# Kernel tuning notes

Measured on AMD Instinct MI355X. Metric: run time of the kernel, lower is better.

The kernel has to match this reference:

```python
import jax, jax.numpy as jnp
import numpy as np
from jax import lax

G = 64      # ngroup
CPN = 4     # channels per group in hidden layers
H, W = 32, 64
K = 5       # conv kernel
BIN = 8     # bin_num
BIAS = 3.5  # (bin_num-1)/2
NMIX = 3    # GMM components (batch replicas)
SCALE = 65536.0


def _group_mask(cout, cin, strict):
    # wavefront causality: tap (dg, di, dj) allowed iff dg+di+dj < 0 (strict) or <= 0
    g = jnp.arange(G)
    dg = g[None, :] - g[:, None]                      # (Gout, Gin)
    off = jnp.arange(K) - K // 2
    dd = off[:, None] + off[None, :]                  # (K, K)
    tot = dg[:, :, None, None] + dd[None, None, :, :]
    m = (tot < 0) if strict else (tot <= 0)
    m = jnp.repeat(jnp.repeat(m, cout, axis=0), cin, axis=1)
    return m.astype(jnp.float32)                      # (G*cout, G*cin, K, K)


def _cconv(x, w, b, m, relu):
    y = lax.conv_general_dilated(x, w * m, (1, 1), 'SAME',
                                 dimension_numbers=('NCHW', 'OIHW', 'NCHW'))
    y = y + b[None, :, None, None]
    return jax.nn.relu(y) if relu else y


def setup_inputs() -> dict:
    key = jax.random.key(0)
    ks = jax.random.split(key, 8)
    data = jax.random.randint(ks[0], (1, G, H, W), 0, BIN).astype(jnp.float32)
    mask = jax.random.randint(ks[1], (1, G, H, W), 0, 2).astype(jnp.float32)
    s = 0.05
    w_in = jax.random.normal(ks[2], (G * CPN, G, K, K), jnp.float32) * s
    b_in = jnp.zeros((G * CPN,), jnp.float32)
    w_hid = jax.random.normal(ks[3], (10, G * CPN, G * CPN, K, K), jnp.float32) * s
    b_hid = jnp.zeros((10, G * CPN), jnp.float32)
    w_out = jax.random.normal(ks[4], (G * NMIX, G * CPN, K, K), jnp.float32) * s
    b_out = jnp.zeros((G * NMIX,), jnp.float32)
    return dict(data=data, mask=mask, w_in=w_in, b_in=b_in,
                w_hid=w_hid, b_hid=b_hid, w_out=w_out, b_out=b_out)


def reference(data, mask, w_in, b_in, w_hid, b_hid, w_out, b_out):
    m_in = _group_mask(CPN, 1, True)      # first layer: strict (excludes current group)
    m_hid = _group_mask(CPN, CPN, False)
    m_out = _group_mask(NMIX, CPN, False)
    tdata = (data - BIAS) * mask
    x = jnp.concatenate([tdata, tdata, tdata], axis=0)   # (3, G, H, W)
    x = _cconv(x, w_in, b_in, m_in, True)
    for i in range(5):                                   # 5 residual blocks
        h = _cconv(x, w_hid[2 * i], b_hid[2 * i], m_hid, True)
        h = _cconv(h, w_hid[2 * i + 1], b_hid[2 * i + 1], m_hid, True)
        x = x + h
    y = _cconv(x, w_out, b_out, m_out, False)            # (3, G*3, H, W)
    y = y.reshape(NMIX, G, NMIX, H, W)                   # batch replica m -> mixture m
    logits = y[:, :, 0]
    mu = y[:, :, 1]
    sig = jax.nn.softplus(y[:, :, 2]) + 1e-6
    wts = jax.nn.softmax(logits, axis=0)                 # (3, G, H, W)
    edges = jnp.arange(BIN, dtype=jnp.float32) + 0.5 - BIAS
    z = (edges[:, None, None, None, None] - mu[None]) / (sig[None] * jnp.float32(np.sqrt(2.0)))
    cdf = 0.5 * (1.0 + lax.erf(z))                       # (BIN, 3, G, H, W)
    table = jnp.einsum('kmghw,mghw->ghwk', cdf, wts) * SCALE
    return table                                         # (G, H, W, BIN) quantizable CDF
```

## Files before the change

### kernel.cpp

```cpp
#include <hip/hip_runtime.h>
#include <math.h>

typedef _Float16 f16;
typedef _Float16 f16x8 __attribute__((ext_vector_type(8)));
typedef float f32x4 __attribute__((ext_vector_type(4)));

#define HH 32
#define WW 64
#define NPX 2048
#define SLOTS 68
#define LOSCALE 2048.0f
#define INV_LOSCALE 4.8828125e-4f

typedef const __attribute__((address_space(1))) void gvoid;
typedef __attribute__((address_space(3))) void lvoid;
__device__ __forceinline__ void gload_lds16(const void* g, void* l) {
    __builtin_amdgcn_global_load_lds((gvoid*)g, (lvoid*)l, 16, 0, 0);
}

__global__ void zero_kernel(f16* p, int n8) {
    int i = blockIdx.x * 256 + threadIdx.x;
    if (i < n8) *(int4*)(p + i * 8) = make_int4(0, 0, 0, 0);
}

__global__ void prep_kernel(const float* __restrict__ data,
                            const float* __restrict__ mask,
                            f16* __restrict__ X0, int plane) {
    int idx = blockIdx.x * 256 + threadIdx.x;
    if (idx >= NPX * 64) return;
    int px = idx >> 6, ci = idx & 63;
    int hh = px >> 6, w = px & 63;
    float v = (data[ci * NPX + px] - 3.5f) * mask[ci * NPX + px];
    int dst = ((hh + 2) * SLOTS + (w + 2)) * 64 + ci;
    X0[dst] = (f16)v;
    X0[plane + dst] = (f16)0.f;
}

__global__ void repack_kernel(const float* __restrict__ W, f16* __restrict__ WP,
                              int cin_log2, int coutp_log2,
                              int cpg_in_log2, int limb, int is_out) {
    int idx = blockIdx.x * 256 + threadIdx.x;
    int Cin = 1 << cin_log2;
    int plane = 25 << (cin_log2 + coutp_log2);
    int ci = idx & (Cin - 1);
    int rest = idx >> cin_log2;
    int co_p = rest & ((1 << coutp_log2) - 1);
    int tap = rest >> coutp_log2;
    if (tap >= 25) return;
    int ky = tap / 5, kx = tap - 5 * ky;
    int co_orig, g_out;
    if (is_out) { g_out = co_p >> 1; co_orig = 3 * g_out + 1 + (co_p & 1); }
    else        { g_out = co_p >> 2; co_orig = co_p; }
    int g_in = ci >> cpg_in_log2;
    float v = 0.f;
    if (ky + kx <= limb + g_out - g_in)
        v = W[(co_orig * Cin + ci) * 25 + tap];
    f16 vh = (f16)v;
    WP[idx] = vh;
    WP[plane + idx] = (f16)((v - (float)vh) * LOSCALE);
}

__global__ __launch_bounds__(320, 3) void conv_kernel(
    const f16* __restrict__ IN, int Cin, int inPlane,
    const f16* __restrict__ WP, int wPlane,
    const float* __restrict__ bias,
    const f16* __restrict__ RES, int resPlane,
    f16* __restrict__ OA, int oaPlane,
    float* __restrict__ OT,
    int nmt, int Coutp, int cpg_out, int cpg_in, int limb, int mode)
{
    __shared__ __align__(16) char SMEM[46080];
    f16* BL = (f16*)SMEM;
    float* RED = (float*)SMEM;

    const int t = threadIdx.x;
    const int kw = t >> 6;
    const int lane = t & 63, l15 = lane & 15, q = lane >> 4;

    int b = blockIdx.x;
    int half = nmt << 4;
    int slot = b >= half ? 1 : 0;
    int idx = b - (slot ? half : 0);
    int mt8 = idx >> 5;
    const int h = idx & 31;
    const int mt = slot ? (nmt - 1 - mt8) : mt8;
    const int co0 = mt * 16;
    const int g_max = (co0 + 15) / cpg_out;

    int cnt[5];
#pragma unroll
    for (int kx = 0; kx < 5; kx++) {
        int c = (g_max + limb - (kw + kx) + 1) * cpg_in;
        c = c < Cin ? c : Cin;
        cnt[kx] = c > 0 ? c : 0;
    }
    int ci_top = (g_max + limb + 1) * cpg_in;
    ci_top = ci_top < Cin ? ci_top : Cin;

    const f16* src[9];
#pragma unroll
    for (int r = 0; r < 9; r++) {
        int u = r * 320 + t;
        if (u >= 2720) u = 0;
        int plane = u / 1360;
        int rem = u - plane * 1360;
        int s4 = rem >> 2;
        int ci16 = rem & 3;
        int row = s4 / 68;
        int slt = s4 - row * 68;
        src[r] = IN + plane * inPlane + ((h + row) * SLOTS + slt) * Cin + ci16 * 8;
    }

    f32x4 acc_h[4], acc_m[4];
#pragma unroll
    for (int j = 0; j < 4; j++) {
        acc_h[j] = (f32x4){0.f, 0.f, 0.f, 0.f};
        acc_m[j] = (f32x4){0.f, 0.f, 0.f, 0.f};
    }

    const size_t kxs = (size_t)Coutp * Cin;

    for (int ci0 = 0; ci0 < ci_top; ci0 += 32) {
        __syncthreads();
#pragma unroll
        for (int r = 0; r < 9; r++) {
            int ub = r * 320 + kw * 64;
            if (ub < 2720)
                gload_lds16(src[r] + ci0, BL + ub * 8);
        }
        __syncthreads();

        const f16* wbase = WP + ((size_t)(kw * 5) * Coutp + co0) * Cin + ci0;
        f16x8 cah, cal, nah, nal;
        if (ci0 < cnt[0]) {
            cah = *(const f16x8*)(wbase + l15 * Cin + q * 8);
            cal = *(const f16x8*)(wbase + wPlane + l15 * Cin + q * 8);
        }
#pragma unroll
        for (int kx = 0; kx < 5; kx++) {
            if (ci0 >= cnt[kx]) break;
            if (kx < 4 && ci0 < cnt[kx + 1]) {
                nah = *(const f16x8*)(wbase + (kx + 1) * kxs + l15 * Cin + q * 8);
                nal = *(const f16x8*)(wbase + (kx + 1) * kxs + wPlane + l15 * Cin + q * 8);
            }
            f16x8 bh[4], bl[4];
#pragma unroll
            for (int j = 0; j < 4; j++) {
                int slt = j * 16 + l15 + kx;
                bh[j] = *(const f16x8*)&BL[(0 * 5 + kw) * (SLOTS * 32) + slt * 32 + q * 8];
                bl[j] = *(const f16x8*)&BL[(1 * 5 + kw) * (SLOTS * 32) + slt * 32 + q * 8];
            }
#pragma unroll
            for (int j = 0; j < 4; j++) {
                acc_h[j] = __builtin_amdgcn_mfma_f32_16x16x32_f16(cah, bh[j], acc_h[j], 0, 0, 0);
                acc_m[j] = __builtin_amdgcn_mfma_f32_16x16x32_f16(cah, bl[j], acc_m[j], 0, 0, 0);
                acc_m[j] = __builtin_amdgcn_mfma_f32_16x16x32_f16(cal, bh[j], acc_m[j], 0, 0, 0);
            }
            cah = nah; cal = nal;
        }
    }

    __syncthreads();
#pragma unroll
    for (int j = 0; j < 4; j++) {
        f32x4 v;
#pragma unroll
        for (int r = 0; r < 4; r++)
            v[r] = acc_h[j][r] + acc_m[j][r] * INV_LOSCALE;
        *(f32x4*)&RED[(kw * 64 + j * 16 + l15) * 20 + q * 4] = v;
    }
    __syncthreads();

    if (mode == 0) {
        for (int c = t; c < 1024; c += 320) {
            int px = c >> 4, col = c & 15;
            float v = bias[co0 + col];
#pragma unroll
            for (int k5 = 0; k5 < 5; k5++) v += RED[(k5 * 64 + px) * 20 + col];
            v = fmaxf(v, 0.f);
            int o = ((h + 2) * SLOTS + px + 2) * Coutp + co0 + col;
            if (RES) v += (float)RES[o] + (float)RES[resPlane + o] * INV_LOSCALE;
            f16 vh = (f16)v;
            OA[o] = vh;
            OA[oaPlane + o] = (f16)((v - (float)vh) * LOSCALE);
        }
    } else {
        for (int c = t; c < 1024; c += 320) {
            int px = c >> 4, col = c & 15;
            float v = bias[3 * ((co0 + col) >> 1) + 1 + (col & 1)];
#pragma unroll
            for (int k5 = 0; k5 < 5; k5++) v += RED[(k5 * 64 + px) * 20 + col];
            RED[px * 20 + col] = v;
        }
        __syncthreads();
        for (int c = t; c < 512; c += 320) {
            int px = c >> 3, gl = c & 7;
            float mu = RED[px * 20 + 2 * gl];
            float s  = RED[px * 20 + 2 * gl + 1];
            float sp = fmaxf(s, 0.f) + log1pf(expf(-fabsf(s)));
            float sig = sp + 1e-6f;
            float inv = 1.f / (sig * 1.41421356237f);
            int g = (co0 >> 1) + gl;
            float* o = OT + ((size_t)g * NPX + h * WW + px) * 8;
#pragma unroll
            for (int k = 0; k < 8; k++) {
                float z = ((float)k - 3.0f - mu) * inv;
                o[k] = 32768.f * (1.f + erff(z));
            }
        }
    }
}

extern "C" void kernel_launch(void* const* d_in, const int* in_sizes, int n_in,
                              void* d_out, int out_size, void* d_ws, size_t ws_size,
                              hipStream_t stream) {
    const float* data  = (const float*)d_in[0];
    const float* mask  = (const float*)d_in[1];
    const float* w_in  = (const float*)d_in[2];
    const float* b_in  = (const float*)d_in[3];
    const float* w_hid = (const float*)d_in[4];
    const float* b_hid = (const float*)d_in[5];
    const float* w_out = (const float*)d_in[6];
    const float* b_out = (const float*)d_in[7];
    float* out = (float*)d_out;

    f16* WP = (f16*)d_ws;
    f16* P  = WP + 3276800;
    f16* Q  = P + 1253376;
    f16* X0 = Q + 1253376;

    zero_kernel<<<1377, 256, 0, stream>>>(P, 352512);
    prep_kernel<<<512, 256, 0, stream>>>(data, mask, X0, 156672);

    repack_kernel<<<1600, 256, 0, stream>>>(w_in, WP, 6, 8, 0, 3, 0);
    conv_kernel<<<512, 320, 0, stream>>>(X0, 64, 156672, WP, 409600,
        b_in, nullptr, 0, P, 626688, nullptr, 16, 256, 4, 1, 3, 0);

    for (int i = 0; i < 5; i++) {
        repack_kernel<<<6400, 256, 0, stream>>>(w_hid + (size_t)(2 * i) * 1638400,
                                                WP, 8, 8, 2, 4, 0);
        conv_kernel<<<512, 320, 0, stream>>>(P, 256, 626688, WP, 1638400,
            b_hid + 2 * i * 256, nullptr, 0, Q, 626688, nullptr, 16, 256, 4, 4, 4, 0);
        repack_kernel<<<6400, 256, 0, stream>>>(w_hid + (size_t)(2 * i + 1) * 1638400,
                                                WP, 8, 8, 2, 4, 0);
        conv_kernel<<<512, 320, 0, stream>>>(Q, 256, 626688, WP, 1638400,
            b_hid + (2 * i + 1) * 256, P, 626688, P, 626688, nullptr, 16, 256, 4, 4, 4, 0);
    }

    repack_kernel<<<3200, 256, 0, stream>>>(w_out, WP, 8, 7, 2, 4, 1);
    conv_kernel<<<256, 320, 0, stream>>>(P, 256, 626688, WP, 819200,
        b_out, nullptr, 0, nullptr, 0, out, 8, 128, 2, 4, 4, 1);
}
```

Baseline: 497.1 us.

## Retile conv to 32x32 output blocks with double-buffered async LDS loads

Each block now computes a tile of 32 output channels by 32 pixels instead of 16 channels by 64 pixels, using a 2x2 grid of MFMA accumulators so every loaded weight and input fragment is reused twice. The input tile loads are double-buffered in LDS with async global-to-LDS loads, waited on with explicit vmcnt counts and raw barriers, so the next channel chunk streams in while the current one is computed. This removes one of the two barriers per iteration. In exchange the kernel uses more LDS, and the occupancy hint drops from 3 to 2 blocks. Causal-mask skipping also gets coarser, since g_max now spans 32 channels.

```diff
diff --git a/kernel.cpp b/kernel.cpp
--- a/kernel.cpp
+++ b/kernel.cpp
@@ -60,7 +60,7 @@
     WP[plane + idx] = (f16)((v - (float)vh) * LOSCALE);
 }
 
-__global__ __launch_bounds__(320, 3) void conv_kernel(
+__global__ __launch_bounds__(320, 2) void conv_kernel(
     const f16* __restrict__ IN, int Cin, int inPlane,
     const f16* __restrict__ WP, int wPlane,
     const float* __restrict__ bias,
@@ -69,7 +69,7 @@
     float* __restrict__ OT,
     int nmt, int Coutp, int cpg_out, int cpg_in, int limb, int mode)
 {
-    __shared__ __align__(16) char SMEM[46080];
+    __shared__ __align__(16) char SMEM[51200];
     f16* BL = (f16*)SMEM;
     float* RED = (float*)SMEM;
 
@@ -78,14 +78,15 @@
     const int lane = t & 63, l15 = lane & 15, q = lane >> 4;
 
     int b = blockIdx.x;
-    int half = nmt << 4;
-    int slot = b >= half ? 1 : 0;
-    int idx = b - (slot ? half : 0);
-    int mt8 = idx >> 5;
+    int half = nmt << 5;
+    int sl = b >= half ? 1 : 0;
+    int idx = b - (sl ? half : 0);
+    int mtRaw = idx >> 5;
     const int h = idx & 31;
-    const int mt = slot ? (nmt - 1 - mt8) : mt8;
-    const int co0 = mt * 16;
-    const int g_max = (co0 + 15) / cpg_out;
+    const int mt = sl ? (nmt - 1 - mtRaw) : mtRaw;
+    const int co0 = mt * 32;
+    const int px0 = sl * 32;
+    const int g_max = (co0 + 31) / cpg_out;
 
     int cnt[5];
 #pragma unroll
@@ -96,89 +97,115 @@
     }
     int ci_top = (g_max + limb + 1) * cpg_in;
     ci_top = ci_top < Cin ? ci_top : Cin;
-
-    const f16* src[9];
-#pragma unroll
-    for (int r = 0; r < 9; r++) {
+    const int NT = (ci_top + 31) >> 5;
+
+    const f16* src[5];
+#pragma unroll
+    for (int r = 0; r < 5; r++) {
         int u = r * 320 + t;
-        if (u >= 2720) u = 0;
-        int plane = u / 1360;
-        int rem = u - plane * 1360;
-        int s4 = rem >> 2;
-        int ci16 = rem & 3;
-        int row = s4 / 68;
-        int slt = s4 - row * 68;
-        src[r] = IN + plane * inPlane + ((h + row) * SLOTS + slt) * Cin + ci16 * 8;
-    }
-
-    f32x4 acc_h[4], acc_m[4];
-#pragma unroll
-    for (int j = 0; j < 4; j++) {
-        acc_h[j] = (f32x4){0.f, 0.f, 0.f, 0.f};
-        acc_m[j] = (f32x4){0.f, 0.f, 0.f, 0.f};
-    }
+        if (u >= 1440) u = 0;
+        int pl = u >= 720 ? 1 : 0;
+        int rem = u - pl * 720;
+        int row = rem / 144;
+        int rr = rem - row * 144;
+        int slt = rr >> 2, c16 = rr & 3;
+        src[r] = IN + (size_t)pl * inPlane
+               + ((h + row) * SLOTS + px0 + slt) * Cin + c16 * 8;
+    }
+
+    f32x4 acc_h[2][2], acc_m[2][2];
+#pragma unroll
+    for (int i = 0; i < 2; i++)
+#pragma unroll
+        for (int j = 0; j < 2; j++) {
+            acc_h[i][j] = (f32x4){0.f, 0.f, 0.f, 0.f};
+            acc_m[i][j] = (f32x4){0.f, 0.f, 0.f, 0.f};
+        }
 
     const size_t kxs = (size_t)Coutp * Cin;
-
-    for (int ci0 = 0; ci0 < ci_top; ci0 += 32) {
-        __syncthreads();
-#pragma unroll
-        for (int r = 0; r < 9; r++) {
-            int ub = r * 320 + kw * 64;
-            if (ub < 2720)
-                gload_lds16(src[r] + ci0, BL + ub * 8);
-        }
-        __syncthreads();
-
-        const f16* wbase = WP + ((size_t)(kw * 5) * Coutp + co0) * Cin + ci0;
-        f16x8 cah, cal, nah, nal;
+    const f16* wb0 = WP + ((size_t)(kw * 5) * Coutp + co0) * Cin + q * 8;
+
+#pragma unroll
+    for (int r = 0; r < 5; r++)
+        gload_lds16(src[r], BL + (r * 320 + kw * 64) * 8);
+
+    for (int it = 0; it < NT; ++it) {
+        const int ci0 = it << 5;
+        f16* buf = BL + (it & 1) * 12800;
+        if (it + 1 < NT) {
+            f16* nb = BL + ((it & 1) ^ 1) * 12800;
+#pragma unroll
+            for (int r = 0; r < 5; r++)
+                gload_lds16(src[r] + ci0 + 32, nb + (r * 320 + kw * 64) * 8);
+            asm volatile("s_waitcnt vmcnt(5)" ::: "memory");
+        } else {
+            asm volatile("s_waitcnt vmcnt(0)" ::: "memory");
+        }
+        __builtin_amdgcn_s_barrier();
+        asm volatile("" ::: "memory");
+
+        const f16* wb = wb0 + ci0;
+        const f16* bhp = buf + kw * 1152 + q * 8;
+        const f16* blp = buf + (5 + kw) * 1152 + q * 8;
+        f16x8 cah0, cah1, cal0, cal1, nah0, nah1, nal0, nal1;
         if (ci0 < cnt[0]) {
-            cah = *(const f16x8*)(wbase + l15 * Cin + q * 8);
-            cal = *(const f16x8*)(wbase + wPlane + l15 * Cin + q * 8);
+            cah0 = *(const f16x8*)(wb + l15 * Cin);
+            cah1 = *(const f16x8*)(wb + (16 + l15) * Cin);
+            cal0 = *(const f16x8*)(wb + wPlane + l15 * Cin);
+            cal1 = *(const f16x8*)(wb + wPlane + (16 + l15) * Cin);
         }
 #pragma unroll
         for (int kx = 0; kx < 5; kx++) {
             if (ci0 >= cnt[kx]) break;
             if (kx < 4 && ci0 < cnt[kx + 1]) {
-                nah = *(const f16x8*)(wbase + (kx + 1) * kxs + l15 * Cin + q * 8);
-                nal = *(const f16x8*)(wbase + (kx + 1) * kxs + wPlane + l15 * Cin + q * 8);
+                const f16* nwb = wb + (kx + 1) * kxs;
+                nah0 = *(const f16x8*)(nwb + l15 * Cin);
+                nah1 = *(const f16x8*)(nwb + (16 + l15) * Cin);
+                nal0 = *(const f16x8*)(nwb + wPlane + l15 * Cin);
+                nal1 = *(const f16x8*)(nwb + wPlane + (16 + l15) * Cin);
             }
-            f16x8 bh[4], bl[4];
-#pragma unroll
-            for (int j = 0; j < 4; j++) {
-                int slt = j * 16 + l15 + kx;
-                bh[j] = *(const f16x8*)&BL[(0 * 5 + kw) * (SLOTS * 32) + slt * 32 + q * 8];
-                bl[j] = *(const f16x8*)&BL[(1 * 5 + kw) * (SLOTS * 32) + slt * 32 + q * 8];
-            }
-#pragma unroll
-            for (int j = 0; j < 4; j++) {
-                acc_h[j] = __builtin_amdgcn_mfma_f32_16x16x32_f16(cah, bh[j], acc_h[j], 0, 0, 0);
-                acc_m[j] = __builtin_amdgcn_mfma_f32_16x16x32_f16(cah, bl[j], acc_m[j], 0, 0, 0);
-                acc_m[j] = __builtin_amdgcn_mfma_f32_16x16x32_f16(cal, bh[j], acc_m[j], 0, 0, 0);
-            }
-            cah = nah; cal = nal;
-        }
-    }
-
-    __syncthreads();
-#pragma unroll
-    for (int j = 0; j < 4; j++) {
-        f32x4 v;
-#pragma unroll
-        for (int r = 0; r < 4; r++)
-            v[r] = acc_h[j][r] + acc_m[j][r] * INV_LOSCALE;
-        *(f32x4*)&RED[(kw * 64 + j * 16 + l15) * 20 + q * 4] = v;
-    }
+            f16x8 bh0 = *(const f16x8*)(bhp + (l15 + kx) * 32);
+            f16x8 bh1 = *(const f16x8*)(bhp + (16 + l15 + kx) * 32);
+            f16x8 bl0 = *(const f16x8*)(blp + (l15 + kx) * 32);
+            f16x8 bl1 = *(const f16x8*)(blp + (16 + l15 + kx) * 32);
+            acc_h[0][0] = __builtin_amdgcn_mfma_f32_16x16x32_f16(cah0, bh0, acc_h[0][0], 0, 0, 0);
+            acc_h[0][1] = __builtin_amdgcn_mfma_f32_16x16x32_f16(cah0, bh1, acc_h[0][1], 0, 0, 0);
+            acc_h[1][0] = __builtin_amdgcn_mfma_f32_16x16x32_f16(cah1, bh0, acc_h[1][0], 0, 0, 0);
+            acc_h[1][1] = __builtin_amdgcn_mfma_f32_16x16x32_f16(cah1, bh1, acc_h[1][1], 0, 0, 0);
+            acc_m[0][0] = __builtin_amdgcn_mfma_f32_16x16x32_f16(cah0, bl0, acc_m[0][0], 0, 0, 0);
+            acc_m[0][1] = __builtin_amdgcn_mfma_f32_16x16x32_f16(cah0, bl1, acc_m[0][1], 0, 0, 0);
+            acc_m[1][0] = __builtin_amdgcn_mfma_f32_16x16x32_f16(cah1, bl0, acc_m[1][0], 0, 0, 0);
+            acc_m[1][1] = __builtin_amdgcn_mfma_f32_16x16x32_f16(cah1, bl1, acc_m[1][1], 0, 0, 0);
+            acc_m[0][0] = __builtin_amdgcn_mfma_f32_16x16x32_f16(cal0, bh0, acc_m[0][0], 0, 0, 0);
+            acc_m[0][1] = __builtin_amdgcn_mfma_f32_16x16x32_f16(cal0, bh1, acc_m[0][1], 0, 0, 0);
+            acc_m[1][0] = __builtin_amdgcn_mfma_f32_16x16x32_f16(cal1, bh0, acc_m[1][0], 0, 0, 0);
+            acc_m[1][1] = __builtin_amdgcn_mfma_f32_16x16x32_f16(cal1, bh1, acc_m[1][1], 0, 0, 0);
+            cah0 = nah0; cah1 = nah1; cal0 = nal0; cal1 = nal1;
+        }
+        __builtin_amdgcn_s_barrier();
+        asm volatile("" ::: "memory");
+    }
+
+#pragma unroll
+    for (int i = 0; i < 2; i++)
+#pragma unroll
+        for (int j = 0; j < 2; j++) {
+            f32x4 v;
+#pragma unroll
+            for (int r = 0; r < 4; r++)
+                v[r] = acc_h[i][j][r] + acc_m[i][j][r] * INV_LOSCALE;
+            *(f32x4*)&RED[(kw * 32 + j * 16 + l15) * 36 + i * 16 + q * 4] = v;
+        }
     __syncthreads();
 
     if (mode == 0) {
         for (int c = t; c < 1024; c += 320) {
-            int px = c >> 4, col = c & 15;
+            int px = c >> 5, col = c & 31;
             float v = bias[co0 + col];
 #pragma unroll
-            for (int k5 = 0; k5 < 5; k5++) v += RED[(k5 * 64 + px) * 20 + col];
+            for (int k5 = 0; k5 < 5; k5++) v += RED[(k5 * 32 + px) * 36 + col];
             v = fmaxf(v, 0.f);
-            int o = ((h + 2) * SLOTS + px + 2) * Coutp + co0 + col;
+            int o = ((h + 2) * SLOTS + px0 + px + 2) * Coutp + co0 + col;
             if (RES) v += (float)RES[o] + (float)RES[resPlane + o] * INV_LOSCALE;
             f16 vh = (f16)v;
             OA[o] = vh;
@@ -186,22 +213,22 @@
         }
     } else {
         for (int c = t; c < 1024; c += 320) {
-            int px = c >> 4, col = c & 15;
+            int px = c >> 5, col = c & 31;
             float v = bias[3 * ((co0 + col) >> 1) + 1 + (col & 1)];
 #pragma unroll
-            for (int k5 = 0; k5 < 5; k5++) v += RED[(k5 * 64 + px) * 20 + col];
-            RED[px * 20 + col] = v;
+            for (int k5 = 0; k5 < 5; k5++) v += RED[(k5 * 32 + px) * 36 + col];
+            RED[px * 36 + col] = v;
         }
         __syncthreads();
         for (int c = t; c < 512; c += 320) {
-            int px = c >> 3, gl = c & 7;
-            float mu = RED[px * 20 + 2 * gl];
-            float s  = RED[px * 20 + 2 * gl + 1];
+            int px = c >> 4, gl = c & 15;
+            float mu = RED[px * 36 + 2 * gl];
+            float s  = RED[px * 36 + 2 * gl + 1];
             float sp = fmaxf(s, 0.f) + log1pf(expf(-fabsf(s)));
             float sig = sp + 1e-6f;
             float inv = 1.f / (sig * 1.41421356237f);
             int g = (co0 >> 1) + gl;
-            float* o = OT + ((size_t)g * NPX + h * WW + px) * 8;
+            float* o = OT + ((size_t)g * NPX + h * WW + px0 + px) * 8;
 #pragma unroll
             for (int k = 0; k < 8; k++) {
                 float z = ((float)k - 3.0f - mu) * inv;
@@ -234,20 +261,20 @@
 
     repack_kernel<<<1600, 256, 0, stream>>>(w_in, WP, 6, 8, 0, 3, 0);
     conv_kernel<<<512, 320, 0, stream>>>(X0, 64, 156672, WP, 409600,
-        b_in, nullptr, 0, P, 626688, nullptr, 16, 256, 4, 1, 3, 0);
+        b_in, nullptr, 0, P, 626688, nullptr, 8, 256, 4, 1, 3, 0);
 
     for (int i = 0; i < 5; i++) {
         repack_kernel<<<6400, 256, 0, stream>>>(w_hid + (size_t)(2 * i) * 1638400,
                                                 WP, 8, 8, 2, 4, 0);
         conv_kernel<<<512, 320, 0, stream>>>(P, 256, 626688, WP, 1638400,
-            b_hid + 2 * i * 256, nullptr, 0, Q, 626688, nullptr, 16, 256, 4, 4, 4, 0);
+            b_hid + 2 * i * 256, nullptr, 0, Q, 626688, nullptr, 8, 256, 4, 4, 4, 0);
         repack_kernel<<<6400, 256, 0, stream>>>(w_hid + (size_t)(2 * i + 1) * 1638400,
                                                 WP, 8, 8, 2, 4, 0);
         conv_kernel<<<512, 320, 0, stream>>>(Q, 256, 626688, WP, 1638400,
-            b_hid + (2 * i + 1) * 256, P, 626688, P, 626688, nullptr, 16, 256, 4, 4, 4, 0);
+            b_hid + (2 * i + 1) * 256, P, 626688, P, 626688, nullptr, 8, 256, 4, 4, 4, 0);
     }
 
     repack_kernel<<<3200, 256, 0, stream>>>(w_out, WP, 8, 7, 2, 4, 1);
     conv_kernel<<<256, 320, 0, stream>>>(P, 256, 626688, WP, 819200,
-        b_out, nullptr, 0, nullptr, 0, out, 8, 128, 2, 4, 4, 1);
-}
+        b_out, nullptr, 0, nullptr, 0, out, 4, 128, 2, 4, 4, 1);
+}
```

Result: slower. 584.2 us (+17.5%).

## Store activations and weights in 32-channel chunked layout for contiguous loads

Applied to the files above, without the earlier changes.

Activations are re-laid out as 32-channel chunks per padded plane (CHS stride), so each per-iteration LDS fill of 5 rows reads one contiguous region instead of strided 64-byte pieces per pixel. Weights are repacked into 16x32 tiles per tap/output-tile/channel-chunk so each wave's fragment load hits one contiguous 1KB block. This also simplifies address arithmetic in the kernel. The trade-off is that the prep, repack, epilogue indexing and every consumer of these buffers must agree on the new layout.

```diff
diff --git a/kernel.cpp b/kernel.cpp
--- a/kernel.cpp
+++ b/kernel.cpp
@@ -9,6 +9,7 @@
 #define WW 64
 #define NPX 2048
 #define SLOTS 68
+#define CHS 78336
 #define LOSCALE 2048.0f
 #define INV_LOSCALE 4.8828125e-4f
 
@@ -31,7 +32,7 @@
     int px = idx >> 6, ci = idx & 63;
     int hh = px >> 6, w = px & 63;
     float v = (data[ci * NPX + px] - 3.5f) * mask[ci * NPX + px];
-    int dst = ((hh + 2) * SLOTS + (w + 2)) * 64 + ci;
+    int dst = (ci >> 5) * CHS + ((hh + 2) * SLOTS + (w + 2)) * 32 + (ci & 31);
     X0[dst] = (f16)v;
     X0[plane + dst] = (f16)0.f;
 }
@@ -56,8 +57,10 @@
     if (ky + kx <= limb + g_out - g_in)
         v = W[(co_orig * Cin + ci) * 25 + tap];
     f16 vh = (f16)v;
-    WP[idx] = vh;
-    WP[plane + idx] = (f16)((v - (float)vh) * LOSCALE);
+    int dst = (((tap << (coutp_log2 - 4)) + (co_p >> 4)) << (cin_log2 - 5 + 9))
+            + ((ci >> 5) << 9) + ((co_p & 15) << 5) + (ci & 31);
+    WP[dst] = vh;
+    WP[plane + dst] = (f16)((v - (float)vh) * LOSCALE);
 }
 
 __global__ __launch_bounds__(320, 3) void conv_kernel(
@@ -102,13 +105,9 @@
     for (int r = 0; r < 9; r++) {
         int u = r * 320 + t;
         if (u >= 2720) u = 0;
-        int plane = u / 1360;
-        int rem = u - plane * 1360;
-        int s4 = rem >> 2;
-        int ci16 = rem & 3;
-        int row = s4 / 68;
-        int slt = s4 - row * 68;
-        src[r] = IN + plane * inPlane + ((h + row) * SLOTS + slt) * Cin + ci16 * 8;
+        int pl = u >= 1360 ? 1 : 0;
+        int rem = u - pl * 1360;
+        src[r] = IN + (size_t)pl * inPlane + h * 2176 + rem * 8;
     }
 
     f32x4 acc_h[4], acc_m[4];
@@ -119,29 +118,32 @@
     }
 
     const size_t kxs = (size_t)Coutp * Cin;
-
-    for (int ci0 = 0; ci0 < ci_top; ci0 += 32) {
+    const f16* wb0 = WP + (size_t)(kw * 5 * (Coutp >> 4) + mt) * ((size_t)Cin << 4)
+                   + l15 * 32 + q * 8;
+
+    int coff = 0;
+    for (int ci0 = 0; ci0 < ci_top; ci0 += 32, coff += CHS) {
         __syncthreads();
 #pragma unroll
         for (int r = 0; r < 9; r++) {
             int ub = r * 320 + kw * 64;
             if (ub < 2720)
-                gload_lds16(src[r] + ci0, BL + ub * 8);
+                gload_lds16(src[r] + coff, BL + ub * 8);
         }
         __syncthreads();
 
-        const f16* wbase = WP + ((size_t)(kw * 5) * Coutp + co0) * Cin + ci0;
+        const f16* wb = wb0 + (ci0 >> 5) * 512;
         f16x8 cah, cal, nah, nal;
         if (ci0 < cnt[0]) {
-            cah = *(const f16x8*)(wbase + l15 * Cin + q * 8);
-            cal = *(const f16x8*)(wbase + wPlane + l15 * Cin + q * 8);
+            cah = *(const f16x8*)(wb);
+            cal = *(const f16x8*)(wb + wPlane);
         }
 #pragma unroll
         for (int kx = 0; kx < 5; kx++) {
             if (ci0 >= cnt[kx]) break;
             if (kx < 4 && ci0 < cnt[kx + 1]) {
-                nah = *(const f16x8*)(wbase + (kx + 1) * kxs + l15 * Cin + q * 8);
-                nal = *(const f16x8*)(wbase + (kx + 1) * kxs + wPlane + l15 * Cin + q * 8);
+                nah = *(const f16x8*)(wb + (kx + 1) * kxs);
+                nal = *(const f16x8*)(wb + (kx + 1) * kxs + wPlane);
             }
             f16x8 bh[4], bl[4];
 #pragma unroll
@@ -178,7 +180,8 @@
 #pragma unroll
             for (int k5 = 0; k5 < 5; k5++) v += RED[(k5 * 64 + px) * 20 + col];
             v = fmaxf(v, 0.f);
-            int o = ((h + 2) * SLOTS + px + 2) * Coutp + co0 + col;
+            int cc = co0 + col;
+            int o = (cc >> 5) * CHS + ((h + 2) * SLOTS + px + 2) * 32 + (cc & 31);
             if (RES) v += (float)RES[o] + (float)RES[resPlane + o] * INV_LOSCALE;
             f16 vh = (f16)v;
             OA[o] = vh;
```

Result: faster. 459.7 us (-7.5%).
